# Kernel optimization log

Measured on AMD Instinct MI355X. Metric: run time of the kernel, lower is better.

## Reference

```python
import jax, jax.numpy as jnp
import numpy as np

HEADS = 4
HEAD_SIZE = 100
SCALE = 1.0 / (100.0 ** 0.5)  # original divides by 100**0.5


def setup_inputs() -> dict:
    key = jax.random.key(0)
    ks = jax.random.split(key, 8)
    B, L, D = 16, 2048, 400
    u0, u1 = 512, 256
    return {
        "x": jax.random.normal(ks[0], (B, L, D), dtype=jnp.float32),
        "kernel": jax.random.normal(ks[1], (3, D, HEAD_SIZE), dtype=jnp.float32) * 0.05,
        "dense": jax.random.normal(ks[2], (D, 400), dtype=jnp.float32) * 0.05,
        "w2": jax.random.normal(ks[3], (400, 400), dtype=jnp.float32) * 0.05,
        "b2": jnp.zeros((400,), dtype=jnp.float32),
        "w3": jax.random.normal(ks[4], (800, u0), dtype=jnp.float32) * 0.05,
        "b3": jnp.zeros((u0,), dtype=jnp.float32),
        "w4": jax.random.normal(ks[5], (u0, u1), dtype=jnp.float32) * 0.05,
        "b4": jnp.zeros((u1,), dtype=jnp.float32),
    }


def reference(x, kernel, dense, w2, b2, w3, b3, w4, b4):
    # --- MultiHeadAttention(4, 100): all heads share the same kernel, so
    # compute one head and tile (identical math to the per-head Python loop).
    q = jnp.einsum("bld,dh->blh", x, kernel[0])  # [B,L,100]
    k = jnp.einsum("bld,dh->blh", x, kernel[1])
    v = jnp.einsum("bld,dh->blh", x, kernel[2])
    scores = jnp.einsum("bqh,bkh->bqk", q, k) * SCALE  # [B,L,L]
    attn = jax.nn.softmax(scores, axis=-1)
    head = jnp.einsum("bqk,bkh->bqh", attn, v)  # [B,L,100]
    out = jnp.concatenate([head] * HEADS, axis=-1)  # [B,L,400]
    out = jnp.einsum("blh,ho->blo", out, dense)  # [B,L,400]
    # Dropout(0.1): identity at inference.
    h = jax.nn.relu(jnp.einsum("blo,ou->blu", out, w2) + b2)  # [B,L,400]
    h_max = jnp.max(h, axis=1)   # GlobalMaxPooling1D -> [B,400]
    h_avg = jnp.mean(h, axis=1)  # GlobalAveragePooling1D -> [B,400]
    z = jnp.concatenate([h_max, h_avg], axis=-1)  # [B,800]
    z = jax.nn.relu(z @ w3 + b3)
    z = jax.nn.relu(z @ w4 + b4)
    return z
```

## Files before the change

kernel.cpp:

```cpp
#include <hip/hip_runtime.h>


#define L_SEQ 2048
#define HS    100
#define ATT_SCALE 0.1f

typedef __attribute__((ext_vector_type(8))) short bf16x8;
typedef __attribute__((ext_vector_type(4))) float f32x4;
#define MFMA16 __builtin_amdgcn_mfma_f32_16x16x32_bf16

__device__ __forceinline__ ushort f2bf(float f) {
    unsigned u = __float_as_uint(f);
    u += 0x7fffu + ((u >> 16) & 1u);
    return (ushort)(u >> 16);
}
__device__ __forceinline__ float bfval(ushort u) {
    return __uint_as_float((unsigned)u << 16);
}

__global__ __launch_bounds__(256)
void k_w(const float* __restrict__ dense, const float* __restrict__ w2,
         ushort* __restrict__ WT_hi, ushort* __restrict__ WT_lo) {
    __shared__ float rows[4 * 400];
    __shared__ float red[4][4][64];
    const int cb = blockIdx.x;
    const int r0 = blockIdx.y * 4;
    const int tid = threadIdx.x;
    const int c = tid & 63, kk = tid >> 6;
    const int col = cb * 64 + c;
    for (int i = tid; i < 1600; i += 256) {
        int rr = r0 + i / 400, cc = i - (i / 400) * 400;
        rows[i] = (rr < 100)
            ? dense[rr * 400 + cc] + dense[(rr + 100) * 400 + cc]
              + dense[(rr + 200) * 400 + cc] + dense[(rr + 300) * 400 + cc]
            : 0.f;
    }
    __syncthreads();
    float a0 = 0.f, a1 = 0.f, a2 = 0.f, a3 = 0.f;
    if (col < 400) {
        const int kbase = kk * 100;
#pragma unroll 4
        for (int k = 0; k < 100; ++k) {
            float wv = w2[(kbase + k) * 400 + col];
            a0 += rows[kbase + k] * wv;
            a1 += rows[400 + kbase + k] * wv;
            a2 += rows[800 + kbase + k] * wv;
            a3 += rows[1200 + kbase + k] * wv;
        }
    }
    red[kk][0][c] = a0; red[kk][1][c] = a1; red[kk][2][c] = a2; red[kk][3][c] = a3;
    __syncthreads();
    {
        const int r = kk;
        float s = red[0][r][c] + red[1][r][c] + red[2][r][c] + red[3][r][c];
        ushort hi = f2bf(s);
        WT_hi[col * 128 + r0 + r] = hi;
        WT_lo[col * 128 + r0 + r] = f2bf(s - bfval(hi));
    }
}

__global__ __launch_bounds__(448)
void k_wprep(const float* __restrict__ kw,
             ushort* __restrict__ wT_hi, ushort* __restrict__ wT_lo) {
    const int j = blockIdx.x;
    const int c = j >> 7, h = j & 127;
    const int k = threadIdx.x;
    float v = 0.f;
    if (h < 100 && k < 400) v = kw[c * 40000 + k * 100 + h];
    if (c == 0) v *= ATT_SCALE;
    ushort hi = f2bf(v);
    wT_hi[(size_t)j * 448 + k] = hi;
    wT_lo[(size_t)j * 448 + k] = f2bf(v - bfval(hi));
}

__global__ __launch_bounds__(512, 2)
void k_qkv(const float* __restrict__ x,
           const ushort* __restrict__ wT_hi, const ushort* __restrict__ wT_lo,
           ushort* __restrict__ q_hi, ushort* __restrict__ q_lo,
           ushort* __restrict__ k_hi, ushort* __restrict__ vT)
{
    __shared__ __align__(16) ushort xh_s[2][128 * 64];
    __shared__ __align__(16) ushort xl_s[2][128 * 64];
    const int row0 = blockIdx.x << 7;
    const int bb = row0 >> 11;
    const int tid = threadIdx.x;
    const int lane = tid & 63, wv = tid >> 6;
    const int q15 = lane & 15, g0 = lane >> 4;
    const int cW = (wv & 3) * 96, rW = (wv >> 2) * 64;

    f32x4 acc[6][4];
#pragma unroll
    for (int mf = 0; mf < 6; ++mf)
#pragma unroll
        for (int nf = 0; nf < 4; ++nf) acc[mf][nf] = (f32x4){0.f, 0.f, 0.f, 0.f};

    float4 st[4];
#define QKV_STAGE_LOAD(KC)                                                     \
    _Pragma("unroll") for (int i = 0; i < 4; ++i) {                            \
        int idx = tid + i * 512; int r = idx >> 4, c4 = idx & 15;              \
        int g = (KC) * 64 + c4 * 4;                                            \
        st[i] = (g <= 396) ? *reinterpret_cast<const float4*>(                 \
                                 &x[(size_t)(row0 + r) * 400 + g])             \
                           : make_float4(0.f, 0.f, 0.f, 0.f);                  \
    }
#define QKV_STAGE_WRITE(BUF)                                                   \
    _Pragma("unroll") for (int i = 0; i < 4; ++i) {                            \
        int idx = tid + i * 512; int r = idx >> 4, c4 = idx & 15;              \
        ushort4 hi4, lo4;                                                      \
        hi4.x = f2bf(st[i].x); lo4.x = f2bf(st[i].x - bfval(hi4.x));           \
        hi4.y = f2bf(st[i].y); lo4.y = f2bf(st[i].y - bfval(hi4.y));           \
        hi4.z = f2bf(st[i].z); lo4.z = f2bf(st[i].z - bfval(hi4.z));           \
        hi4.w = f2bf(st[i].w); lo4.w = f2bf(st[i].w - bfval(hi4.w));           \
        int off = r * 128 + ((c4 * 8) ^ ((r & 7) << 4));                       \
        *reinterpret_cast<ushort4*>((char*)xh_s[BUF] + off) = hi4;             \
        *reinterpret_cast<ushort4*>((char*)xl_s[BUF] + off) = lo4;             \
    }

    QKV_STAGE_LOAD(0)

    for (int kc = 0; kc < 7; ++kc) {
        const int cur = kc & 1;
        QKV_STAGE_WRITE(cur)
        if (kc < 6) { QKV_STAGE_LOAD(kc + 1) }
        __syncthreads();
#pragma unroll
        for (int k2 = 0; k2 < 2; ++k2) {
            const int k0 = kc * 64 + k2 * 32;
            bf16x8 bh[4], bl[4];
#pragma unroll
            for (int nf = 0; nf < 4; ++nf) {
                int row = rW + nf * 16 + q15;
                int boff = row * 128 + ((k2 * 64 + g0 * 16) ^ ((row & 7) << 4));
                bh[nf] = *reinterpret_cast<const bf16x8*>((char*)xh_s[cur] + boff);
                bl[nf] = *reinterpret_cast<const bf16x8*>((char*)xl_s[cur] + boff);
            }
#pragma unroll
            for (int mf = 0; mf < 6; ++mf) {
                int col = cW + mf * 16 + q15;
                bf16x8 ah = *reinterpret_cast<const bf16x8*>(
                    wT_hi + (size_t)col * 448 + k0 + g0 * 8);
                bf16x8 al = *reinterpret_cast<const bf16x8*>(
                    wT_lo + (size_t)col * 448 + k0 + g0 * 8);
#pragma unroll
                for (int nf = 0; nf < 4; ++nf) {
                    acc[mf][nf] = MFMA16(ah, bh[nf], acc[mf][nf], 0, 0, 0);
                    acc[mf][nf] = MFMA16(ah, bl[nf], acc[mf][nf], 0, 0, 0);
                    acc[mf][nf] = MFMA16(al, bh[nf], acc[mf][nf], 0, 0, 0);
                }
            }
        }
    }

#pragma unroll
    for (int mf = 0; mf < 6; ++mf) {
        const int col0 = cW + mf * 16 + 4 * g0;
        const int c = col0 >> 7, h0 = col0 & 127;
#pragma unroll
        for (int nf = 0; nf < 4; ++nf) {
            const size_t row = (size_t)(row0 + rW + nf * 16 + q15);
            if (c == 0) {
                ushort4 hi4, lo4;
#pragma unroll
                for (int r = 0; r < 4; ++r) {
                    float vf = acc[mf][nf][r];
                    ushort h = f2bf(vf);
                    ((ushort*)&hi4)[r] = h;
                    ((ushort*)&lo4)[r] = f2bf(vf - bfval(h));
                }
                *reinterpret_cast<ushort4*>(&q_hi[row * 128 + h0]) = hi4;
                *reinterpret_cast<ushort4*>(&q_lo[row * 128 + h0]) = lo4;
            } else if (c == 1) {
                ushort4 hi4;
#pragma unroll
                for (int r = 0; r < 4; ++r) ((ushort*)&hi4)[r] = f2bf(acc[mf][nf][r]);
                *reinterpret_cast<ushort4*>(&k_hi[row * 128 + h0]) = hi4;
            } else {
                const int keyl = (int)row & 2047;
#pragma unroll
                for (int jj = 0; jj < 4; ++jj) {
                    int h = h0 + jj;
                    if (h < 100)
                        vT[((size_t)bb * 112 + h) * 2048 + keyl] = f2bf(acc[mf][nf][jj]);
                }
            }
        }
    }
#undef QKV_STAGE_LOAD
#undef QKV_STAGE_WRITE
}

template<bool PART>
__global__ __launch_bounds__(256, 4)
void k_flashT(const ushort* __restrict__ q_hi, const ushort* __restrict__ q_lo,
              const ushort* __restrict__ k_hi, const ushort* __restrict__ vT,
              float* __restrict__ outp, float2* __restrict__ mlP)
{
    __shared__ __align__(16) ushort k_s[64 * 128];
    __shared__ __align__(16) ushort vT_s[112 * 64];
    __shared__ __align__(16) ushort p_s[4][16 * 64];

    const int id = blockIdx.x;
    int b, qt, part;
    if (PART) {
        const int Lg = (id & 7) * 128 + (id >> 3);
        b = Lg >> 6; const int rem = Lg & 63; qt = rem >> 1; part = rem & 1;
    } else {
        const int Lg = (id & 7) * 64 + (id >> 3);
        b = Lg >> 5; qt = Lg & 31; part = 0;
    }
    const int q0 = qt * 64;
    const size_t bL = (size_t)b * L_SEQ;
    const int ktBeg = part * 16, ktEnd = PART ? ktBeg + 16 : 32;

    const int tid = threadIdx.x;
    const int lane = tid & 63, wv = tid >> 6;
    const int q15 = lane & 15, g0 = lane >> 4;

    bf16x8 qhf[4], qlf[4];
    {
        const ushort* qr = q_hi + (bL + q0 + 16 * wv + q15) * 128 + 8 * g0;
        const ushort* qs = q_lo + (bL + q0 + 16 * wv + q15) * 128 + 8 * g0;
#pragma unroll
        for (int kh = 0; kh < 4; ++kh) {
            qhf[kh] = *reinterpret_cast<const bf16x8*>(qr + 32 * kh);
            qlf[kh] = *reinterpret_cast<const bf16x8*>(qs + 32 * kh);
        }
    }

    float m_run = -1e30f, l_run = 0.f;
    f32x4 acc[7];
#pragma unroll
    for (int ht = 0; ht < 7; ++ht) acc[ht] = (f32x4){0.f, 0.f, 0.f, 0.f};

    for (int kt = ktBeg; kt < ktEnd; ++kt) {
        const int kb = kt * 64;
        __syncthreads();
        {
            const char* khg = (const char*)(k_hi + (bL + kb) * 128);
            for (int n = tid; n < 1024; n += 256) {
                int key = n >> 4, gg = n & 15;
                uint4 d = *reinterpret_cast<const uint4*>(khg + n * 16);
                *reinterpret_cast<uint4*>((char*)k_s + key * 256 + (((gg ^ (key & 15))) << 4)) = d;
            }
            const char* vtg = (const char*)(vT + (size_t)b * 112 * 2048) + kb * 2;
            for (int n = tid; n < 896; n += 256) {
                int h = n >> 3, gg = n & 7;
                uint4 d = *reinterpret_cast<const uint4*>(vtg + h * 4096 + gg * 16);
                *reinterpret_cast<uint4*>((char*)vT_s + h * 128 + (((gg ^ (h & 7))) << 4)) = d;
            }
        }
        __syncthreads();

        f32x4 sacc[4];
        const int kx = q15 << 4;
#pragma unroll
        for (int t = 0; t < 4; ++t) {
            sacc[t] = (f32x4){0.f, 0.f, 0.f, 0.f};
            const char* kr = (const char*)k_s + (t * 16 + q15) * 256;
#pragma unroll
            for (int kh = 0; kh < 4; ++kh) {
                bf16x8 kf = *reinterpret_cast<const bf16x8*>(kr + ((((kh << 2) + g0) << 4) ^ kx));
                sacc[t] = MFMA16(kf, qhf[kh], sacc[t], 0, 0, 0);
                sacc[t] = MFMA16(kf, qlf[kh], sacc[t], 0, 0, 0);
            }
        }

        float mxl = -1e30f;
#pragma unroll
        for (int t = 0; t < 4; ++t)
#pragma unroll
            for (int r = 0; r < 4; ++r) mxl = fmaxf(mxl, sacc[t][r]);
        mxl = fmaxf(mxl, __shfl_xor(mxl, 16));
        mxl = fmaxf(mxl, __shfl_xor(mxl, 32));
        if (!__all(mxl - m_run <= 8.f)) {
            float mn = fmaxf(m_run, mxl);
            float alpha = __expf(m_run - mn);
            l_run *= alpha;
            m_run = mn;
            float alv[4];
#pragma unroll
            for (int r = 0; r < 4; ++r) alv[r] = __shfl(alpha, (g0 << 2) | r);
#pragma unroll
            for (int ht = 0; ht < 7; ++ht)
#pragma unroll
                for (int r = 0; r < 4; ++r) acc[ht][r] *= alv[r];
        }
        float lsum = 0.f;
        float p[4][4];
#pragma unroll
        for (int t = 0; t < 4; ++t)
#pragma unroll
            for (int r = 0; r < 4; ++r) {
                p[t][r] = __expf(sacc[t][r] - m_run);
                lsum += p[t][r];
            }
        lsum += __shfl_xor(lsum, 16);
        lsum += __shfl_xor(lsum, 32);
        l_run += lsum;

        ushort* pw = p_s[wv];
        const int qb = q15 * 128;
#pragma unroll
        for (int t = 0; t < 4; ++t) {
            ushort4 pv4;
            pv4.x = f2bf(p[t][0]); pv4.y = f2bf(p[t][1]);
            pv4.z = f2bf(p[t][2]); pv4.w = f2bf(p[t][3]);
            int gw = (t << 1) + (g0 >> 1);
            *reinterpret_cast<ushort4*>((char*)pw + qb + (((gw ^ (q15 & 7))) << 4)
                                        + ((g0 & 1) << 3)) = pv4;
        }

        bf16x8 pa0 = *reinterpret_cast<const bf16x8*>((char*)pw + qb + (((g0 ^ (q15 & 7))) << 4));
        bf16x8 pa1 = *reinterpret_cast<const bf16x8*>((char*)pw + qb + ((((4 + g0) ^ (q15 & 7))) << 4));
#pragma unroll
        for (int ht = 0; ht < 7; ++ht) {
            const char* vr = (const char*)vT_s + (ht * 16 + q15) * 128;
            const int hx = ((ht * 16 + q15) & 7) << 4;
            bf16x8 vb0 = *reinterpret_cast<const bf16x8*>(vr + ((g0 << 4) ^ hx));
            bf16x8 vb1 = *reinterpret_cast<const bf16x8*>(vr + (((4 + g0) << 4) ^ hx));
            acc[ht] = MFMA16(pa0, vb0, acc[ht], 0, 0, 0);
            acc[ht] = MFMA16(pa1, vb1, acc[ht], 0, 0, 0);
        }
    }

    if (PART) {
        float* ap = outp + (size_t)part * 3276800
                    + (bL + q0 + 16 * wv + (g0 << 2)) * 100;
#pragma unroll
        for (int ht = 0; ht < 7; ++ht) {
            int col = ht * 16 + q15;
            if (col < 100) {
#pragma unroll
                for (int r = 0; r < 4; ++r) ap[r * 100 + col] = acc[ht][r];
            }
        }
        if (g0 == 0) {
            float2 ml; ml.x = m_run; ml.y = l_run;
            mlP[(size_t)part * 32768 + bL + q0 + 16 * wv + q15] = ml;
        }
    } else {
        float linv[4];
#pragma unroll
        for (int r = 0; r < 4; ++r) linv[r] = 1.0f / __shfl(l_run, (g0 << 2) | r);
#pragma unroll
        for (int ht = 0; ht < 7; ++ht) {
            int col = ht * 16 + q15;
            if (col < 100) {
                float* hp = outp + (bL + q0 + 16 * wv + (g0 << 2)) * 100 + col;
#pragma unroll
                for (int r = 0; r < 4; ++r) hp[r * 100] = acc[ht][r] * linv[r];
            }
        }
    }
}

__global__ __launch_bounds__(256)
void k_combine(float* __restrict__ accP, const float2* __restrict__ mlP)
{
    int g = blockIdx.x * 256 + threadIdx.x;
    if (g < 32768 * 25) {
        int row = g / 25, c4 = g - row * 25;
        float2 ml1 = mlP[row], ml2 = mlP[32768 + row];
        float M = fmaxf(ml1.x, ml2.x);
        float w1 = __expf(ml1.x - M), w2 = __expf(ml2.x - M);
        float inv = 1.0f / (w1 * ml1.y + w2 * ml2.y);
        float4 a1 = *reinterpret_cast<const float4*>(&accP[(size_t)row * 100 + c4 * 4]);
        float4 a2 = *reinterpret_cast<const float4*>(&accP[3276800 + (size_t)row * 100 + c4 * 4]);
        float4 o;
        o.x = (w1 * a1.x + w2 * a2.x) * inv;
        o.y = (w1 * a1.y + w2 * a2.y) * inv;
        o.z = (w1 * a1.z + w2 * a2.z) * inv;
        o.w = (w1 * a1.w + w2 * a2.w) * inv;
        *reinterpret_cast<float4*>(&accP[(size_t)row * 100 + c4 * 4]) = o;
    }
}

__global__ __launch_bounds__(512, 2)
void k_hpool(const float* __restrict__ head,
             const ushort* __restrict__ WT_hi, const ushort* __restrict__ WT_lo,
             const float* __restrict__ b2,
             float* __restrict__ pmax, float* __restrict__ psum)
{
    __shared__ __align__(16) ushort hh_s[128 * 128];
    __shared__ __align__(16) ushort hl_s[128 * 128];
    __shared__ float pm_s[8][112], ps_s[8][112];
    const int blk = blockIdx.x;
    const int row0 = blk << 7;
    const int tid = threadIdx.x;
    const int lane = tid & 63, wv = tid >> 6;
    const int q15 = lane & 15, g0 = lane >> 4;
    const int wvM = wv >> 2, wvN = wv & 3;

    for (int i = 0; i < 7; ++i) {
        int idx = tid + i * 512;
        if (idx < 3200) {
            int r = idx / 25, cc = idx - r * 25;
            float4 t = *reinterpret_cast<const float4*>(
                &head[(size_t)(row0 + r) * 100 + cc * 4]);
            ushort4 hi4, lo4;
            hi4.x = f2bf(t.x); lo4.x = f2bf(t.x - bfval(hi4.x));
            hi4.y = f2bf(t.y); lo4.y = f2bf(t.y - bfval(hi4.y));
            hi4.z = f2bf(t.z); lo4.z = f2bf(t.z - bfval(hi4.z));
            hi4.w = f2bf(t.w); lo4.w = f2bf(t.w - bfval(hi4.w));
            int off = r * 256 + ((cc * 8) ^ ((r & 7) << 4));
            *reinterpret_cast<ushort4*>((char*)hh_s + off) = hi4;
            *reinterpret_cast<ushort4*>((char*)hl_s + off) = lo4;
        }
    }
    for (int idx = tid; idx < 896; idx += 512) {
        int r = idx / 7, c7 = idx - (idx / 7) * 7;
        int off = r * 256 + (((200 + c7 * 8)) ^ ((r & 7) << 4));
        ushort4 z = {0, 0, 0, 0};
        *reinterpret_cast<ushort4*>((char*)hh_s + off) = z;
        *reinterpret_cast<ushort4*>((char*)hl_s + off) = z;
    }
    __syncthreads();

    f32x4 acc[4][7];
#pragma unroll
    for (int mf = 0; mf < 4; ++mf)
#pragma unroll
        for (int nf = 0; nf < 7; ++nf) acc[mf][nf] = (f32x4){0.f, 0.f, 0.f, 0.f};

#pragma unroll
    for (int ks = 0; ks < 4; ++ks) {
        const int k0 = ks * 32;
        bf16x8 ah[4], al[4];
#pragma unroll
        for (int mf = 0; mf < 4; ++mf) {
            int rowL = wvM * 64 + mf * 16 + q15;
            int aoff = rowL * 256 + ((k0 * 2 + g0 * 16) ^ ((rowL & 7) << 4));
            ah[mf] = *reinterpret_cast<const bf16x8*>((char*)hh_s + aoff);
            al[mf] = *reinterpret_cast<const bf16x8*>((char*)hl_s + aoff);
        }
#pragma unroll
        for (int nf = 0; nf < 7; ++nf) {
            int col = wvN * 112 + nf * 16 + q15;
            bf16x8 bh = *reinterpret_cast<const bf16x8*>(WT_hi + col * 128 + k0 + g0 * 8);
            bf16x8 bl = *reinterpret_cast<const bf16x8*>(WT_lo + col * 128 + k0 + g0 * 8);
#pragma unroll
            for (int mf = 0; mf < 4; ++mf) {
                acc[mf][nf] = MFMA16(ah[mf], bh, acc[mf][nf], 0, 0, 0);
                acc[mf][nf] = MFMA16(ah[mf], bl, acc[mf][nf], 0, 0, 0);
                acc[mf][nf] = MFMA16(al[mf], bh, acc[mf][nf], 0, 0, 0);
            }
        }
    }

#pragma unroll
    for (int nf = 0; nf < 7; ++nf) {
        int col = wvN * 112 + nf * 16 + q15;
        float bv = (col < 400) ? b2[col] : 0.f;
        float mx = 0.f, sm = 0.f;
#pragma unroll
        for (int mf = 0; mf < 4; ++mf)
#pragma unroll
            for (int r = 0; r < 4; ++r) {
                float hv = fmaxf(acc[mf][nf][r] + bv, 0.f);
                mx = fmaxf(mx, hv); sm += hv;
            }
        mx = fmaxf(mx, __shfl_xor(mx, 16));
        mx = fmaxf(mx, __shfl_xor(mx, 32));
        sm += __shfl_xor(sm, 16);
        sm += __shfl_xor(sm, 32);
        if (g0 == 0) {
            pm_s[wv][nf * 16 + q15] = mx;
            ps_s[wv][nf * 16 + q15] = sm;
        }
    }
    __syncthreads();
    if (tid < 448) {
        int wn = tid / 112, cc = tid - wn * 112;
        float mx = fmaxf(pm_s[wn][cc], pm_s[4 + wn][cc]);
        float sm = ps_s[wn][cc] + ps_s[4 + wn][cc];
        if (tid < 400) {
            pmax[blk * 400 + tid] = mx;
            psum[blk * 400 + tid] = sm;
        }
    }
}

__global__ __launch_bounds__(512)
void k_reduce(const float* __restrict__ pmax, const float* __restrict__ psum,
              float* __restrict__ zin)
{
    const int b = blockIdx.x, c = threadIdx.x;
    if (c < 400) {
        float m = 0.f, s = 0.f;
#pragma unroll
        for (int tt = 0; tt < 16; ++tt) {
            m = fmaxf(m, pmax[(b * 16 + tt) * 400 + c]);
            s += psum[(b * 16 + tt) * 400 + c];
        }
        zin[b * 800 + c] = m;
        zin[b * 800 + 400 + c] = s * (1.0f / 2048.0f);
    }
}

__global__ __launch_bounds__(512)
void k_mlp1(const float* __restrict__ zin, const float* __restrict__ w3,
            const float* __restrict__ b3, float* __restrict__ z1)
{
    __shared__ float zs[800];
    __shared__ float red[8][64];
    const int cb = blockIdx.x, b = blockIdx.y;
    const int tid = threadIdx.x;
    const int c = tid & 63, kk = tid >> 6;
    const int col = cb * 64 + c;
    for (int i = tid; i < 800; i += 512) zs[i] = zin[b * 800 + i];
    __syncthreads();
    float acc = 0.f;
    const int k0 = kk * 100;
#pragma unroll 4
    for (int k = 0; k < 100; ++k)
        acc += zs[k0 + k] * w3[(k0 + k) * 512 + col];
    red[kk][c] = acc;
    __syncthreads();
    if (kk == 0) {
        float a = b3[col];
#pragma unroll
        for (int g = 0; g < 8; ++g) a += red[g][c];
        z1[b * 512 + col] = fmaxf(a, 0.f);
    }
}

__global__ __launch_bounds__(512)
void k_mlp2(const float* __restrict__ z1, const float* __restrict__ w4,
            const float* __restrict__ b4, float* __restrict__ out)
{
    __shared__ float zs[512];
    __shared__ float red[8][64];
    const int cb = blockIdx.x, b = blockIdx.y;
    const int tid = threadIdx.x;
    const int c = tid & 63, kk = tid >> 6;
    const int col = cb * 64 + c;
    if (tid < 512) zs[tid] = z1[b * 512 + tid];
    __syncthreads();
    float acc = 0.f;
    const int k0 = kk * 64;
#pragma unroll 4
    for (int k = 0; k < 64; ++k)
        acc += zs[k0 + k] * w4[(k0 + k) * 256 + col];
    red[kk][c] = acc;
    __syncthreads();
    if (kk == 0) {
        float a = b4[col];
#pragma unroll
        for (int g = 0; g < 8; ++g) a += red[g][c];
        out[b * 256 + col] = fmaxf(a, 0.f);
    }
}

extern "C" void kernel_launch(void* const* d_in, const int* in_sizes, int n_in,
                              void* d_out, int out_size, void* d_ws, size_t ws_size,
                              hipStream_t stream) {
    (void)in_sizes; (void)n_in; (void)out_size;
    const float* x     = (const float*)d_in[0];
    const float* kw    = (const float*)d_in[1];
    const float* dense = (const float*)d_in[2];
    const float* w2    = (const float*)d_in[3];
    const float* b2    = (const float*)d_in[4];
    const float* w3    = (const float*)d_in[5];
    const float* b3    = (const float*)d_in[6];
    const float* w4    = (const float*)d_in[7];
    const float* b4    = (const float*)d_in[8];
    float* ws = (float*)d_ws;
    ushort* q_hi = (ushort*)(ws);
    ushort* q_lo = (ushort*)(ws + 2097152);
    ushort* k_hi = (ushort*)(ws + 4194304);
    ushort* vT   = (ushort*)(ws + 6291456);
    float*  head = ws + 8126464;
    ushort* wT_hi = (ushort*)(ws + 8126464);
    ushort* wT_lo = (ushort*)(ws + 8212480);
    float*  pmax = ws;
    float*  psum = ws + 2097152;
    float*  zin  = ws + 4194304;
    float*  z1   = ws + 4207104;
    float*  outp = (float*)d_out;

    const bool split = ws_size >= (size_t)14999552 * sizeof(float);
    float*  accP  = head;
    float2* mlP   = (float2*)(ws + 14680064);
    ushort* WT_hi = (ushort*)(ws + (split ? 14942208 : 11403264));
    ushort* WT_lo = WT_hi + 57344;

    k_w     <<<dim3(7, 32),    dim3(256), 0, stream>>>(dense, w2, WT_hi, WT_lo);
    k_wprep <<<dim3(384),      dim3(448), 0, stream>>>(kw, wT_hi, wT_lo);
    k_qkv   <<<dim3(256),      dim3(512), 0, stream>>>(x, wT_hi, wT_lo,
                                                       q_hi, q_lo, k_hi, vT);
    if (split) {
        k_flashT<true> <<<dim3(1024), dim3(256), 0, stream>>>(q_hi, q_lo, k_hi, vT,
                                                              accP, mlP);
        k_combine      <<<dim3(3200), dim3(256), 0, stream>>>(accP, mlP);
    } else {
        k_flashT<false><<<dim3(512),  dim3(256), 0, stream>>>(q_hi, q_lo, k_hi, vT,
                                                              head, nullptr);
    }
    k_hpool <<<dim3(256),      dim3(512), 0, stream>>>(head, WT_hi, WT_lo, b2,
                                                       pmax, psum);
    k_reduce<<<dim3(16),       dim3(512), 0, stream>>>(pmax, psum, zin);
    k_mlp1  <<<dim3(8, 16),    dim3(512), 0, stream>>>(zin, w3, b3, z1);
    k_mlp2  <<<dim3(4, 16),    dim3(512), 0, stream>>>(z1, w4, b4, outp);
}
```

Before: 197.0 us.

## Prefetch next K/V tile into registers during attention compute; reorder QKV staging

```diff
diff --git a/kernel.cpp b/kernel.cpp
--- a/kernel.cpp
+++ b/kernel.cpp
@@ -117,12 +117,12 @@
     }
 
     QKV_STAGE_LOAD(0)
+    QKV_STAGE_WRITE(0)
+    __syncthreads();
 
     for (int kc = 0; kc < 7; ++kc) {
         const int cur = kc & 1;
-        QKV_STAGE_WRITE(cur)
         if (kc < 6) { QKV_STAGE_LOAD(kc + 1) }
-        __syncthreads();
 #pragma unroll
         for (int k2 = 0; k2 < 2; ++k2) {
             const int k0 = kc * 64 + k2 * 32;
@@ -148,6 +148,10 @@
                     acc[mf][nf] = MFMA16(al, bh[nf], acc[mf][nf], 0, 0, 0);
                 }
             }
+        }
+        if (kc < 6) {
+            QKV_STAGE_WRITE(cur ^ 1)
+            __syncthreads();
         }
     }
 
@@ -227,32 +231,53 @@
         }
     }
 
+    uint4 kreg[4], vreg[4];
+#define FL_LOAD(KT_)                                                           \
+    {                                                                          \
+        const char* khg = (const char*)(k_hi + (bL + (KT_) * 64) * 128);       \
+        _Pragma("unroll") for (int i = 0; i < 4; ++i)                          \
+            kreg[i] = *reinterpret_cast<const uint4*>(khg + (tid + i * 256) * 16); \
+        const char* vtg = (const char*)(vT + (size_t)b * 112 * 2048) + (KT_) * 128; \
+        _Pragma("unroll") for (int i = 0; i < 4; ++i) {                        \
+            int n = tid + i * 256;                                             \
+            if (n < 896) {                                                     \
+                int h = n >> 3, gg = n & 7;                                    \
+                vreg[i] = *reinterpret_cast<const uint4*>(vtg + h * 4096 + gg * 16); \
+            }                                                                  \
+        }                                                                      \
+    }
+#define FL_WRITE()                                                             \
+    {                                                                          \
+        _Pragma("unroll") for (int i = 0; i < 4; ++i) {                        \
+            int n = tid + i * 256; int key = n >> 4, gg = n & 15;              \
+            *reinterpret_cast<uint4*>((char*)k_s + key * 256                   \
+                                      + ((gg ^ (key & 15)) << 4)) = kreg[i];   \
+        }                                                                      \
+        _Pragma("unroll") for (int i = 0; i < 4; ++i) {                        \
+            int n = tid + i * 256;                                             \
+            if (n < 896) {                                                     \
+                int h = n >> 3, gg = n & 7;                                    \
+                *reinterpret_cast<uint4*>((char*)vT_s + h * 128                \
+                                          + ((gg ^ (h & 7)) << 4)) = vreg[i];  \
+            }                                                                  \
+        }                                                                      \
+    }
+
     float m_run = -1e30f, l_run = 0.f;
     f32x4 acc[7];
 #pragma unroll
     for (int ht = 0; ht < 7; ++ht) acc[ht] = (f32x4){0.f, 0.f, 0.f, 0.f};
 
+    FL_LOAD(ktBeg)
+    FL_WRITE()
+    __syncthreads();
+
     for (int kt = ktBeg; kt < ktEnd; ++kt) {
-        const int kb = kt * 64;
-        __syncthreads();
-        {
-            const char* khg = (const char*)(k_hi + (bL + kb) * 128);
-            for (int n = tid; n < 1024; n += 256) {
-                int key = n >> 4, gg = n & 15;
-                uint4 d = *reinterpret_cast<const uint4*>(khg + n * 16);
-                *reinterpret_cast<uint4*>((char*)k_s + key * 256 + (((gg ^ (key & 15))) << 4)) = d;
-            }
-            const char* vtg = (const char*)(vT + (size_t)b * 112 * 2048) + kb * 2;
-            for (int n = tid; n < 896; n += 256) {
-                int h = n >> 3, gg = n & 7;
-                uint4 d = *reinterpret_cast<const uint4*>(vtg + h * 4096 + gg * 16);
-                *reinterpret_cast<uint4*>((char*)vT_s + h * 128 + (((gg ^ (h & 7))) << 4)) = d;
-            }
-        }
-        __syncthreads();
+        if (kt + 1 < ktEnd) FL_LOAD(kt + 1)
 
         f32x4 sacc[4];
         const int kx = q15 << 4;
+        __builtin_amdgcn_s_setprio(1);
 #pragma unroll
         for (int t = 0; t < 4; ++t) {
             sacc[t] = (f32x4){0.f, 0.f, 0.f, 0.f};
@@ -264,6 +289,7 @@
                 sacc[t] = MFMA16(kf, qlf[kh], sacc[t], 0, 0, 0);
             }
         }
+        __builtin_amdgcn_s_setprio(0);
 
         float mxl = -1e30f;
 #pragma unroll
@@ -312,6 +338,7 @@
 
         bf16x8 pa0 = *reinterpret_cast<const bf16x8*>((char*)pw + qb + (((g0 ^ (q15 & 7))) << 4));
         bf16x8 pa1 = *reinterpret_cast<const bf16x8*>((char*)pw + qb + ((((4 + g0) ^ (q15 & 7))) << 4));
+        __builtin_amdgcn_s_setprio(1);
 #pragma unroll
         for (int ht = 0; ht < 7; ++ht) {
             const char* vr = (const char*)vT_s + (ht * 16 + q15) * 128;
@@ -321,6 +348,13 @@
             acc[ht] = MFMA16(pa0, vb0, acc[ht], 0, 0, 0);
             acc[ht] = MFMA16(pa1, vb1, acc[ht], 0, 0, 0);
         }
+        __builtin_amdgcn_s_setprio(0);
+
+        if (kt + 1 < ktEnd) {
+            __syncthreads();
+            FL_WRITE()
+            __syncthreads();
+        }
     }
 
     if (PART) {
@@ -352,6 +386,8 @@
             }
         }
     }
+#undef FL_LOAD
+#undef FL_WRITE
 }
 
 __global__ __launch_bounds__(256)
```

Result: slower. 273.9 us (+39.0%).
